# Kernel optimization log

Measured on AMD Instinct MI355X. Metric: run time of the kernel, lower is better.

## Reference

```python
import jax, jax.numpy as jnp
import numpy as np

B, C, H, W = 128, 512, 14, 14
P = 512  # num_parts (codebook size)


def setup_inputs() -> dict:
    key = jax.random.key(0)
    k1, k2, k3 = jax.random.split(key, 3)
    fm = jax.random.normal(k1, (B, C, H, W), dtype=jnp.float32)
    embedding = jax.random.normal(k2, (B, C), dtype=jnp.float32)
    # self.w = torch.randn(P, C).clamp_(min=0)
    w = jnp.maximum(jax.random.normal(k3, (P, C), dtype=jnp.float32), 0.0)
    w_ep_sum = w  # clone of w at init
    w_ep_num = jnp.ones((P,), dtype=jnp.float32)
    return {"fm": fm, "embedding": embedding, "w": w,
            "w_ep_sum": w_ep_sum, "w_ep_num": w_ep_num, "epoch": 5}


def reference(fm, embedding, w, w_ep_sum, w_ep_num, epoch):
    b, c, h, wd = fm.shape
    p = w.shape[0]
    # NCHW -> [B, HW, C]
    x = jnp.transpose(fm, (0, 2, 3, 1)).reshape(b, h * wd, c)
    xf = x.reshape(b * h * wd, c)
    dist = (jnp.sum(xf * xf, axis=1, keepdims=True)
            + jnp.sum(w * w, axis=1)
            - 2.0 * (xf @ w.T))                      # [B*HW, P]
    assign = jax.nn.softmax(-dist.reshape(b, h * wd, p), axis=-1)
    # hard threshold: zero out weak assignments
    assign = jnp.where(assign < 1.0 / p, 0.0, assign)  # [B, HW, P]
    assign_sum = assign.mean(axis=1)                    # [B, P]

    if epoch > 2:  # epoch is a static Python int
        # relu(einsum('bn,nc->bnc').mean(1)) == relu((assign_sum @ w) / P)
        cvec = jax.nn.relu((assign_sum @ w) / p)        # [B, C]
        embedding_cat = jnp.concatenate([embedding, cvec], axis=-1)
    else:
        embedding_cat = jnp.concatenate([embedding, jnp.zeros_like(embedding)], axis=-1)

    # collect_weight (no-grad EMA-style accumulate).
    # einsum('bmn,bmc->bmnc').sum(1).sum(0) == einsum('bmn,bmc->nc') -- avoids
    # materializing the [B,M,N,C] tensor the torch code builds.
    update_w = jnp.einsum('bmn,bmc->nc', assign, x)     # [P, C]
    assign_mean = jnp.sum(assign, axis=(0, 1))          # [P]
    upd = assign_mean > 1.0
    new_w_ep_sum = jnp.where(upd[:, None], w_ep_sum + update_w, w_ep_sum)
    new_w_ep_num = jnp.where(upd, w_ep_num + assign_mean, w_ep_num)
    return embedding_cat, new_w_ep_sum, new_w_ep_num
```

## Files before the change

### kernel.cpp

```cpp
#include <hip/hip_runtime.h>
#include <hip/hip_bf16.h>

#define Bn   128
#define Cn   512
#define HWn  196
#define Mn   25088
#define Pn   512
#define SPLITK2 32
#define KCH  1024

#define OFF_XT     0u
#define OFF_AT     8388608u
#define OFF_PART   16777216u
#define OFF_XM     16777216u
#define OFF_WF     25165824u
#define OFF_WNORM  25296896u
#define OFF_RAWP   25297408u
#define OFF_MEAN   25428480u

#define OUT_CAT  0u
#define OUT_WSUM 131072u
#define OUT_WNUM 393216u

using bf16x8 = __attribute__((ext_vector_type(8))) short;
using f16x8  = __attribute__((ext_vector_type(8))) _Float16;
using f32x4  = __attribute__((ext_vector_type(4))) float;

__device__ __forceinline__ unsigned short f2b(float f) {
    union { float f; unsigned u; } x; x.f = f;
    unsigned r = x.u + 0x7fffu + ((x.u >> 16) & 1u);
    return (unsigned short)(r >> 16);
}
__device__ __forceinline__ float b2f(unsigned short u) {
    union { unsigned u; float f; } x; x.u = ((unsigned)u) << 16;
    return x.f;
}

__global__ __launch_bounds__(64) void k_wnorm(const float* __restrict__ w,
                                              float* __restrict__ wn,
                                              _Float16* __restrict__ wf) {
    int n = blockIdx.x, l = threadIdx.x;
    const float* p = w + (size_t)n * Cn + l * 8;
    float4 a = *(const float4*)p;
    float4 b = *(const float4*)(p + 4);
    float s = a.x*a.x + a.y*a.y + a.z*a.z + a.w*a.w
            + b.x*b.x + b.y*b.y + b.z*b.z + b.w*b.w;
    alignas(16) _Float16 h[8];
    h[0]=(_Float16)a.x; h[1]=(_Float16)a.y; h[2]=(_Float16)a.z; h[3]=(_Float16)a.w;
    h[4]=(_Float16)b.x; h[5]=(_Float16)b.y; h[6]=(_Float16)b.z; h[7]=(_Float16)b.w;
    *(float4*)(wf + (size_t)(n >> 4) * 8192u + (size_t)(l >> 2) * 512
                 + (n & 15) * 32 + (l & 3) * 8) = *(const float4*)h;
    #pragma unroll
    for (int o = 32; o > 0; o >>= 1) s += __shfl_down(s, o);
    if (l == 0) wn[n] = s;
}

__global__ __launch_bounds__(512) void k_prep2(const float* __restrict__ fm,
                                               _Float16* __restrict__ xm,
                                               unsigned short* __restrict__ xt) {
    __shared__ _Float16 tile[64][200];
    int b = blockIdx.x;
    int cg = blockIdx.y * 64;
    int t = threadIdx.x;
    for (int i = t; i < 64 * 49; i += 512) {
        int cl = i / 49, h4 = i - cl * 49;
        float4 v = *(const float4*)(fm + ((size_t)(b * Cn + cg + cl) * HWn) + h4 * 4);
        tile[cl][h4*4+0] = (_Float16)v.x;
        tile[cl][h4*4+1] = (_Float16)v.y;
        tile[cl][h4*4+2] = (_Float16)v.z;
        tile[cl][h4*4+3] = (_Float16)v.w;
    }
    __syncthreads();
    for (int i = t; i < HWn * 8; i += 512) {
        int hw = i >> 3, seg = i & 7;
        alignas(16) _Float16 h[8];
        #pragma unroll
        for (int j = 0; j < 8; ++j) h[j] = tile[seg * 8 + j][hw];
        *(float4*)(xm + (size_t)(b * HWn + hw) * Cn + cg + seg * 8) = *(const float4*)h;
    }
    for (int i = t; i < 64 * 4 * 16; i += 512) {
        int cl = i >> 6, rem = i & 63;
        int q = rem >> 4, j4 = rem & 15;
        ushort4 o;
        if (j4 < 12) {
            o.x = f2b((float)tile[cl][q*49 + j4*4 + 0]);
            o.y = f2b((float)tile[cl][q*49 + j4*4 + 1]);
            o.z = f2b((float)tile[cl][q*49 + j4*4 + 2]);
            o.w = f2b((float)tile[cl][q*49 + j4*4 + 3]);
        } else if (j4 == 12) {
            o.x = f2b((float)tile[cl][q*49 + 48]);
            o.y = 0; o.z = 0; o.w = 0;
        } else {
            o.x = 0; o.y = 0; o.z = 0; o.w = 0;
        }
        int c = cg + cl;
        int T = c >> 4;
        int seg = b * 8 + q * 2 + (j4 >> 3);
        int k = (j4 & 7) * 4;
        *(ushort4*)(xt + (size_t)T * 524288u + (size_t)seg * 512 + (c & 15) * 32 + k) = o;
    }
}

__global__ __launch_bounds__(512) void k_post(const _Float16* __restrict__ xm,
                                              const _Float16* __restrict__ wf,
                                              const float* __restrict__ wnorm,
                                              unsigned short* __restrict__ at,
                                              float* __restrict__ rawp) {
    __shared__ _Float16 As[113][520];
    __shared__ float red[2][64][4];
    __shared__ float colp[2][512];
    const int bid = blockIdx.x;
    const int b = bid >> 1, half = bid & 1;
    const int tid = threadIdx.x;
    const int wave = tid >> 6, lane = tid & 63;
    const int mq = wave >> 2, nq = wave & 3;
    const int rl = lane & 15, rq = lane >> 4;
    const int kb = rq * 8;
    const int m0 = b * 196 + half * 98;
    const int n0 = nq * 128;

    for (int i = tid; i < 113 * 64; i += 512) {
        int row = i >> 6, kc = (i & 63) * 8;
        *(f16x8*)&As[row][kc] = *(const f16x8*)(xm + (size_t)(m0 + row) * Cn + kc);
    }
    __syncthreads();

    const _Float16* wtb = wf + (size_t)(nq * 8) * 8192u + rl * 32 + kb;

    f32x4 acc[4][8] = {};
    for (int seg = 0; seg < 16; ++seg) {
        f16x8 a[4], bb[8];
        #pragma unroll
        for (int f = 0; f < 4; ++f)
            a[f] = *(const f16x8*)&As[mq * 49 + f * 16 + rl][seg * 32 + kb];
        #pragma unroll
        for (int g = 0; g < 8; ++g)
            bb[g] = *(const f16x8*)(wtb + (size_t)g * 8192u + seg * 512);
        #pragma unroll
        for (int f = 0; f < 4; ++f)
            #pragma unroll
            for (int g = 0; g < 8; ++g)
                acc[f][g] = __builtin_amdgcn_mfma_f32_16x16x32_f16(a[f], bb[g], acc[f][g], 0, 0, 0);
    }
    float wn[8];
    #pragma unroll
    for (int g = 0; g < 8; ++g) wn[g] = wnorm[n0 + g * 16 + rl];
    #pragma unroll
    for (int f = 0; f < 4; ++f)
        #pragma unroll
        for (int g = 0; g < 8; ++g)
            #pragma unroll
            for (int r = 0; r < 4; ++r)
                acc[f][g][r] = 2.0f * acc[f][g][r] - wn[g];
    float mx[4][4];
    #pragma unroll
    for (int f = 0; f < 4; ++f)
        #pragma unroll
        for (int r = 0; r < 4; ++r) {
            float m_ = acc[f][0][r];
            #pragma unroll
            for (int g = 1; g < 8; ++g) m_ = fmaxf(m_, acc[f][g][r]);
            #pragma unroll
            for (int o = 8; o >= 1; o >>= 1) m_ = fmaxf(m_, __shfl_xor(m_, o));
            mx[f][r] = m_;
        }
    if (rl == 0)
        #pragma unroll
        for (int f = 0; f < 4; ++f)
            #pragma unroll
            for (int r = 0; r < 4; ++r)
                red[mq][f * 16 + rq * 4 + r][nq] = mx[f][r];
    __syncthreads();
    float rmax[4][4];
    #pragma unroll
    for (int f = 0; f < 4; ++f)
        #pragma unroll
        for (int r = 0; r < 4; ++r) {
            float* q = red[mq][f * 16 + rq * 4 + r];
            rmax[f][r] = fmaxf(fmaxf(q[0], q[1]), fmaxf(q[2], q[3]));
        }
    float sm[4][4];
    #pragma unroll
    for (int f = 0; f < 4; ++f)
        #pragma unroll
        for (int r = 0; r < 4; ++r) {
            float s_ = 0.f;
            #pragma unroll
            for (int g = 0; g < 8; ++g) {
                float p = __expf(acc[f][g][r] - rmax[f][r]);
                acc[f][g][r] = p;
                s_ += p;
            }
            #pragma unroll
            for (int o = 8; o >= 1; o >>= 1) s_ += __shfl_xor(s_, o);
            sm[f][r] = s_;
        }
    __syncthreads();
    if (rl == 0)
        #pragma unroll
        for (int f = 0; f < 4; ++f)
            #pragma unroll
            for (int r = 0; r < 4; ++r)
                red[mq][f * 16 + rq * 4 + r][nq] = sm[f][r];
    __syncthreads();
    const float invP = 1.0f / 512.0f;
    #pragma unroll
    for (int f = 0; f < 4; ++f)
        #pragma unroll
        for (int r = 0; r < 4; ++r) {
            float* q = red[mq][f * 16 + rq * 4 + r];
            float inv = 1.0f / (q[0] + q[1] + q[2] + q[3]);
            #pragma unroll
            for (int g = 0; g < 8; ++g) {
                float a = acc[f][g][r] * inv;
                acc[f][g][r] = (a < invP) ? 0.0f : a;
            }
        }
    float cs[8] = {};
    #pragma unroll
    for (int g = 0; g < 8; ++g) {
        #pragma unroll
        for (int f = 0; f < 4; ++f)
            #pragma unroll
            for (int r = 0; r < 4; ++r)
                if (f * 16 + rq * 4 + r < 49) cs[g] += acc[f][g][r];
        cs[g] += __shfl_xor(cs[g], 16);
        cs[g] += __shfl_xor(cs[g], 32);
    }
    if (rq == 0)
        #pragma unroll
        for (int g = 0; g < 8; ++g) colp[mq][n0 + g * 16 + rl] = cs[g];
    __syncthreads();
    if (tid < 512) rawp[(size_t)bid * 512 + tid] = colp[0][tid] + colp[1][tid];
    const int mb = b * 256 + (half * 2 + mq) * 64;
    const int segbase = mb >> 5;
    #pragma unroll
    for (int f = 0; f < 4; ++f) {
        const int mloc = f * 16 + rq * 4;
        const int seg = segbase + (mloc >> 5);
        const int k = mloc & 31;
        #pragma unroll
        for (int g = 0; g < 8; ++g) {
            ushort4 o;
            o.x = (mloc + 0 < 49) ? f2b(acc[f][g][0]) : (unsigned short)0;
            o.y = (mloc + 1 < 49) ? f2b(acc[f][g][1]) : (unsigned short)0;
            o.z = (mloc + 2 < 49) ? f2b(acc[f][g][2]) : (unsigned short)0;
            o.w = (mloc + 3 < 49) ? f2b(acc[f][g][3]) : (unsigned short)0;
            const int T = nq * 8 + g;
            *(ushort4*)(at + (size_t)T * 524288u + (size_t)seg * 512 + rl * 32 + k) = o;
        }
    }
}

__global__ __launch_bounds__(256) void k_reduce(const float* __restrict__ rawp,
                                                const float* __restrict__ wnum,
                                                float* __restrict__ mean,
                                                float* __restrict__ outnum) {
    int n = blockIdx.x * 256 + threadIdx.x;
    float s = 0.f;
    for (int r = 0; r < 256; ++r) s += rawp[(size_t)r * Pn + n];
    mean[n] = s;
    outnum[n] = wnum[n] + (s > 1.0f ? s : 0.0f);
}

__global__ __launch_bounds__(256) void k_cvec(const float* __restrict__ rawp,
                                              const float* __restrict__ w,
                                              const float* __restrict__ emb,
                                              const int* __restrict__ epoch,
                                              float* __restrict__ out) {
    __shared__ float srow[512];
    int b = blockIdx.x, t = threadIdx.x;
    srow[t]       = rawp[(size_t)(2*b) * Pn + t]       + rawp[(size_t)(2*b+1) * Pn + t];
    srow[t + 256] = rawp[(size_t)(2*b) * Pn + t + 256] + rawp[(size_t)(2*b+1) * Pn + t + 256];
    __syncthreads();
    float a0 = 0.f, a1 = 0.f;
    for (int p = 0; p < Pn; ++p) {
        float ap = srow[p];
        a0 = fmaf(ap, w[(size_t)p * Cn + t], a0);
        a1 = fmaf(ap, w[(size_t)p * Cn + t + 256], a1);
    }
    const float sc = 1.0f / (196.0f * 512.0f);
    int ep = epoch[0];
    float c0 = (ep > 2) ? fmaxf(a0, 0.f) * sc : 0.f;
    float c1 = (ep > 2) ? fmaxf(a1, 0.f) * sc : 0.f;
    out[(size_t)b * 1024 + t]             = emb[(size_t)b * Cn + t];
    out[(size_t)b * 1024 + t + 256]       = emb[(size_t)b * Cn + t + 256];
    out[(size_t)b * 1024 + 512 + t]       = c0;
    out[(size_t)b * 1024 + 512 + t + 256] = c1;
}

__global__ __launch_bounds__(256) void k_upw_mfma(const unsigned short* __restrict__ at,
                                                  const unsigned short* __restrict__ xt,
                                                  unsigned short* __restrict__ part) {
    const int id = blockIdx.x;
    const int sp = id & 31;
    const int m  = id >> 5;
    const int tid = threadIdx.x;
    const int wave = tid >> 6, lane = tid & 63;
    const int wn = wave >> 1, wc = wave & 1;
    const int n0 = (m & 3) * 128;
    const int c0 = (m >> 2) * 128;
    const int rl = lane & 15, rq = lane >> 4;
    const int loff = rl * 32 + rq * 8;
    const int segbase = sp * 32;

    const unsigned short* pa[4];
    const unsigned short* pb[4];
    #pragma unroll
    for (int f = 0; f < 4; ++f) {
        const int Ta = (n0 >> 4) + wn * 4 + f;
        const int Tb = (c0 >> 4) + wc * 4 + f;
        pa[f] = at + (size_t)Ta * 524288u + (size_t)segbase * 512 + loff;
        pb[f] = xt + (size_t)Tb * 524288u + (size_t)segbase * 512 + loff;
    }

    f32x4 acc[4][4] = {};
    bf16x8 aC[4], bC[4], aN[4], bN[4];
    #pragma unroll
    for (int f = 0; f < 4; ++f) {
        aC[f] = *(const bf16x8*)(pa[f]);
        bC[f] = *(const bf16x8*)(pb[f]);
    }
    for (int ks = 0; ks < 32; ks += 2) {
        #pragma unroll
        for (int f = 0; f < 4; ++f) {
            aN[f] = *(const bf16x8*)(pa[f] + (ks + 1) * 512);
            bN[f] = *(const bf16x8*)(pb[f] + (ks + 1) * 512);
        }
        #pragma unroll
        for (int i = 0; i < 4; ++i)
            #pragma unroll
            for (int j = 0; j < 4; ++j)
                acc[i][j] = __builtin_amdgcn_mfma_f32_16x16x32_bf16(aC[i], bC[j], acc[i][j], 0, 0, 0);
        if (ks + 2 < 32) {
            #pragma unroll
            for (int f = 0; f < 4; ++f) {
                aC[f] = *(const bf16x8*)(pa[f] + (ks + 2) * 512);
                bC[f] = *(const bf16x8*)(pb[f] + (ks + 2) * 512);
            }
        }
        #pragma unroll
        for (int i = 0; i < 4; ++i)
            #pragma unroll
            for (int j = 0; j < 4; ++j)
                acc[i][j] = __builtin_amdgcn_mfma_f32_16x16x32_bf16(aN[i], bN[j], acc[i][j], 0, 0, 0);
    }
    unsigned short* o = part + (size_t)sp * (Pn * Cn);
    const int rq4 = rq * 4;
    #pragma unroll
    for (int i = 0; i < 4; ++i) {
        #pragma unroll
        for (int j = 0; j < 4; ++j) {
            int n = n0 + wn * 64 + i * 16 + rq4;
            int c = c0 + wc * 64 + j * 16 + rl;
            #pragma unroll
            for (int r = 0; r < 4; ++r)
                o[(size_t)(n + r) * Cn + c] = f2b(acc[i][j][r]);
        }
    }
}

__global__ __launch_bounds__(256) void k_wep(const unsigned short* __restrict__ part,
                                             const float* __restrict__ mean,
                                             const float* __restrict__ wsum,
                                             float* __restrict__ out1) {
    int n = blockIdx.x, t = threadIdx.x;
    bool upd = mean[n] > 1.0f;
    int c = t * 2;
    float s0 = 0.f, s1 = 0.f;
    #pragma unroll
    for (int k = 0; k < SPLITK2; ++k) {
        ushort2 v = *(const ushort2*)(part + (size_t)k * (Pn * Cn) + (size_t)n * Cn + c);
        s0 += b2f(v.x);
        s1 += b2f(v.y);
    }
    size_t idx = (size_t)n * Cn + c;
    out1[idx]     = wsum[idx]     + (upd ? s0 : 0.f);
    out1[idx + 1] = wsum[idx + 1] + (upd ? s1 : 0.f);
}

extern "C" void kernel_launch(void* const* d_in, const int* in_sizes, int n_in,
                              void* d_out, int out_size, void* d_ws, size_t ws_size,
                              hipStream_t stream) {
    const float* fm    = (const float*)d_in[0];
    const float* emb   = (const float*)d_in[1];
    const float* w     = (const float*)d_in[2];
    const float* wsum  = (const float*)d_in[3];
    const float* wnum  = (const float*)d_in[4];
    const int*   epoch = (const int*)d_in[5];
    float* out = (float*)d_out;
    float* wsf = (float*)d_ws;

    unsigned short* xtb   = (unsigned short*)(wsf + OFF_XT);
    unsigned short* atb   = (unsigned short*)(wsf + OFF_AT);
    unsigned short* partb = (unsigned short*)(wsf + OFF_PART);
    _Float16*       xmb   = (_Float16*)(wsf + OFF_XM);
    _Float16*       wfb   = (_Float16*)(wsf + OFF_WF);
    float*          wnormb = wsf + OFF_WNORM;
    float*          rawpb  = wsf + OFF_RAWP;
    float*          meanb  = wsf + OFF_MEAN;

    k_wnorm<<<512, 64, 0, stream>>>(w, wnormb, wfb);
    k_prep2<<<dim3(Bn, 8), 512, 0, stream>>>(fm, xmb, xtb);
    k_post<<<256, 512, 0, stream>>>(xmb, wfb, wnormb, atb, rawpb);
    k_reduce<<<2, 256, 0, stream>>>(rawpb, wnum, meanb, out + OUT_WNUM);
    k_cvec<<<Bn, 256, 0, stream>>>(rawpb, w, emb, epoch, out + OUT_CAT);
    k_upw_mfma<<<512, 256, 0, stream>>>(atb, xtb, partb);
    k_wep<<<Pn, 256, 0, stream>>>(partb, meanb, wsum, out + OUT_WSUM);
}
```

Baseline: 148.1 us.

## Fuse NCHW transpose/convert prep kernel into distance-softmax kernel

Removes the separate prep kernel that transposed fm into an fp16 row-major buffer and a bf16 tiled buffer. The distance kernel now reads fm directly from NCHW, converts it into shared memory, and writes the bf16 tiled copy for the update GEMM from that shared tile. This drops one launch and the round trip of the fp16 intermediate through global memory. In exchange the fm loads are strided per channel, with lanes reading consecutive hw positions, and the workspace offsets are repacked.

```diff
diff --git a/kernel.cpp b/kernel.cpp
--- a/kernel.cpp
+++ b/kernel.cpp
@@ -12,11 +12,10 @@
 #define OFF_XT     0u
 #define OFF_AT     8388608u
 #define OFF_PART   16777216u
-#define OFF_XM     16777216u
-#define OFF_WF     25165824u
-#define OFF_WNORM  25296896u
-#define OFF_RAWP   25297408u
-#define OFF_MEAN   25428480u
+#define OFF_WF     20971520u
+#define OFF_WNORM  21102592u
+#define OFF_RAWP   21103104u
+#define OFF_MEAN   21234176u
 
 #define OUT_CAT  0u
 #define OUT_WSUM 131072u
@@ -55,56 +54,11 @@
     if (l == 0) wn[n] = s;
 }
 
-__global__ __launch_bounds__(512) void k_prep2(const float* __restrict__ fm,
-                                               _Float16* __restrict__ xm,
-                                               unsigned short* __restrict__ xt) {
-    __shared__ _Float16 tile[64][200];
-    int b = blockIdx.x;
-    int cg = blockIdx.y * 64;
-    int t = threadIdx.x;
-    for (int i = t; i < 64 * 49; i += 512) {
-        int cl = i / 49, h4 = i - cl * 49;
-        float4 v = *(const float4*)(fm + ((size_t)(b * Cn + cg + cl) * HWn) + h4 * 4);
-        tile[cl][h4*4+0] = (_Float16)v.x;
-        tile[cl][h4*4+1] = (_Float16)v.y;
-        tile[cl][h4*4+2] = (_Float16)v.z;
-        tile[cl][h4*4+3] = (_Float16)v.w;
-    }
-    __syncthreads();
-    for (int i = t; i < HWn * 8; i += 512) {
-        int hw = i >> 3, seg = i & 7;
-        alignas(16) _Float16 h[8];
-        #pragma unroll
-        for (int j = 0; j < 8; ++j) h[j] = tile[seg * 8 + j][hw];
-        *(float4*)(xm + (size_t)(b * HWn + hw) * Cn + cg + seg * 8) = *(const float4*)h;
-    }
-    for (int i = t; i < 64 * 4 * 16; i += 512) {
-        int cl = i >> 6, rem = i & 63;
-        int q = rem >> 4, j4 = rem & 15;
-        ushort4 o;
-        if (j4 < 12) {
-            o.x = f2b((float)tile[cl][q*49 + j4*4 + 0]);
-            o.y = f2b((float)tile[cl][q*49 + j4*4 + 1]);
-            o.z = f2b((float)tile[cl][q*49 + j4*4 + 2]);
-            o.w = f2b((float)tile[cl][q*49 + j4*4 + 3]);
-        } else if (j4 == 12) {
-            o.x = f2b((float)tile[cl][q*49 + 48]);
-            o.y = 0; o.z = 0; o.w = 0;
-        } else {
-            o.x = 0; o.y = 0; o.z = 0; o.w = 0;
-        }
-        int c = cg + cl;
-        int T = c >> 4;
-        int seg = b * 8 + q * 2 + (j4 >> 3);
-        int k = (j4 & 7) * 4;
-        *(ushort4*)(xt + (size_t)T * 524288u + (size_t)seg * 512 + (c & 15) * 32 + k) = o;
-    }
-}
-
-__global__ __launch_bounds__(512) void k_post(const _Float16* __restrict__ xm,
+__global__ __launch_bounds__(512) void k_post(const float* __restrict__ fm,
                                               const _Float16* __restrict__ wf,
                                               const float* __restrict__ wnorm,
                                               unsigned short* __restrict__ at,
+                                              unsigned short* __restrict__ xt,
                                               float* __restrict__ rawp) {
     __shared__ _Float16 As[113][520];
     __shared__ float red[2][64][4];
@@ -119,9 +73,19 @@
     const int m0 = b * 196 + half * 98;
     const int n0 = nq * 128;
 
-    for (int i = tid; i < 113 * 64; i += 512) {
-        int row = i >> 6, kc = (i & 63) * 8;
-        *(f16x8*)&As[row][kc] = *(const f16x8*)(xm + (size_t)(m0 + row) * Cn + kc);
+    {
+        const int cg = tid >> 6;
+        int m1 = m0 + lane;        if (m1 > Mn - 1) m1 = Mn - 1;
+        int m2 = m0 + lane + 64;   if (m2 > Mn - 1) m2 = Mn - 1;
+        const int b1 = m1 / HWn, h1 = m1 - b1 * HWn;
+        const int b2 = m2 / HWn, h2 = m2 - b2 * HWn;
+        const float* f1 = fm + (size_t)b1 * (Cn * HWn) + h1;
+        const float* f2 = fm + (size_t)b2 * (Cn * HWn) + h2;
+        const bool ok2 = (lane + 64) < 113;
+        for (int c = cg; c < Cn; c += 8) {
+            As[lane][c] = (_Float16)f1[(size_t)c * HWn];
+            if (ok2) As[lane + 64][c] = (_Float16)f2[(size_t)c * HWn];
+        }
     }
     __syncthreads();
 
@@ -249,6 +213,27 @@
             const int T = nq * 8 + g;
             *(ushort4*)(at + (size_t)T * 524288u + (size_t)seg * 512 + rl * 32 + k) = o;
         }
+    }
+    for (int i = tid; i < 512 * 32; i += 512) {
+        const int c = i >> 5;
+        const int g4 = (i & 31) << 2;
+        const int ch = g4 >> 6;
+        const int mloc = g4 & 63;
+        const int lr = ch * 49 + mloc;
+        ushort4 o;
+        if (mloc < 48) {
+            o.x = f2b((float)As[lr][c]);
+            o.y = f2b((float)As[lr + 1][c]);
+            o.z = f2b((float)As[lr + 2][c]);
+            o.w = f2b((float)As[lr + 3][c]);
+        } else if (mloc == 48) {
+            o.x = f2b((float)As[lr][c]); o.y = 0; o.z = 0; o.w = 0;
+        } else {
+            o.x = 0; o.y = 0; o.z = 0; o.w = 0;
+        }
+        const int seg = b * 8 + (half * 2 + ch) * 2 + (mloc >> 5);
+        *(ushort4*)(xt + (size_t)(c >> 4) * 524288u + (size_t)seg * 512
+                    + (c & 15) * 32 + (mloc & 31)) = o;
     }
 }
 
@@ -394,15 +379,13 @@
     unsigned short* xtb   = (unsigned short*)(wsf + OFF_XT);
     unsigned short* atb   = (unsigned short*)(wsf + OFF_AT);
     unsigned short* partb = (unsigned short*)(wsf + OFF_PART);
-    _Float16*       xmb   = (_Float16*)(wsf + OFF_XM);
     _Float16*       wfb   = (_Float16*)(wsf + OFF_WF);
     float*          wnormb = wsf + OFF_WNORM;
     float*          rawpb  = wsf + OFF_RAWP;
     float*          meanb  = wsf + OFF_MEAN;
 
     k_wnorm<<<512, 64, 0, stream>>>(w, wnormb, wfb);
-    k_prep2<<<dim3(Bn, 8), 512, 0, stream>>>(fm, xmb, xtb);
-    k_post<<<256, 512, 0, stream>>>(xmb, wfb, wnormb, atb, rawpb);
+    k_post<<<256, 512, 0, stream>>>(fm, wfb, wnormb, atb, xtb, rawpb);
     k_reduce<<<2, 256, 0, stream>>>(rawpb, wnum, meanb, out + OUT_WNUM);
     k_cvec<<<Bn, 256, 0, stream>>>(rawpb, w, emb, epoch, out + OUT_CAT);
     k_upw_mfma<<<512, 256, 0, stream>>>(atb, xtb, partb);
```

Result: slower. 165.7 us (+11.9%).
